# Kernel optimization log

Measured on AMD Instinct MI355X. Metric: run time of the kernel, lower is better.

The kernel has to match this reference:

```python
import jax, jax.numpy as jnp
import numpy as np

HEADS = 8
DIM_HEAD = 64


def setup_inputs() -> dict:
    key = jax.random.key(0)
    ks = jax.random.split(key, 7)
    b, c, h, w = 8, 256, 64, 64
    hidden = HEADS * DIM_HEAD  # 512
    return {
        "x": jax.random.normal(ks[0], (b, c, h, w), dtype=jnp.float32),
        "context": jax.random.normal(ks[1], (b, c, h, w), dtype=jnp.float32),
        "Wq": jax.random.normal(ks[2], (hidden, c), dtype=jnp.float32) * 0.02,
        "Wk": jax.random.normal(ks[3], (hidden, c), dtype=jnp.float32) * 0.02,
        "Wv": jax.random.normal(ks[4], (hidden, c), dtype=jnp.float32) * 0.02,
        "Wo": jax.random.normal(ks[5], (c, hidden), dtype=jnp.float32) * 0.02,
        "bo": jnp.zeros((c,), dtype=jnp.float32),
    }


def reference(x, context, Wq, Wk, Wv, Wo, bo):
    b, c, h, w = x.shape
    n = h * w
    scale = DIM_HEAD ** (-0.5)
    xf = x.reshape(b, c, n)                      # b c n
    cf = context.reshape(b, context.shape[1], -1)  # b c m
    # 1x1 convs == per-pixel linear projections
    q = jnp.einsum('bcn,oc->bon', xf, Wq).reshape(b, HEADS, DIM_HEAD, n) * scale
    k = jnp.einsum('bcm,oc->bom', cf, Wk).reshape(b, HEADS, DIM_HEAD, -1)
    v = jnp.einsum('bcm,oc->bom', cf, Wv).reshape(b, HEADS, DIM_HEAD, -1)
    k = jax.nn.softmax(k, axis=-1)               # softmax over spatial positions
    ctx = jnp.einsum('bhdm,bhem->bhde', k, v)    # small d x e context
    out = jnp.einsum('bhde,bhdn->bhen', ctx, q)  # b h e n
    out = out.reshape(b, HEADS * DIM_HEAD, h, w)
    return jnp.einsum('bchw,oc->bohw', out, Wo) + bo[None, :, None, None]
```

## Files before the change

kernel.cpp:

```cpp
#include <hip/hip_runtime.h>

#define B   8
#define C   256
#define N   4096
#define H   8
#define D   64
#define HID 512
#define SCALE 0.125f

typedef __attribute__((ext_vector_type(8))) __bf16 bf16x8;
typedef __attribute__((ext_vector_type(4))) float f32x4;

__device__ __forceinline__ ushort f2bf(float f) {
  union { float f; unsigned u; } v; v.f = f;
  unsigned r = v.u + 0x7FFFu + ((v.u >> 16) & 1u);
  return (ushort)(r >> 16);
}

__device__ __forceinline__ f32x4 mfma16(bf16x8 a, bf16x8 b, f32x4 c) {
  return __builtin_amdgcn_mfma_f32_16x16x32_bf16(a, b, c, 0, 0, 0);
}

__device__ __forceinline__ void glds16(const ushort* g, ushort* l) {
  __builtin_amdgcn_global_load_lds(
      (const __attribute__((address_space(1))) void*)g,
      (__attribute__((address_space(3))) void*)l, 16, 0, 0);
}

__global__ __launch_bounds__(256) void prep_kernel(
    const float* __restrict__ x, const float* __restrict__ ctxt,
    const float* __restrict__ Wk, const float* __restrict__ Wv,
    ushort* __restrict__ x_bf, ushort* __restrict__ ctxt_bf,
    ushort* __restrict__ wk_bf, ushort* __restrict__ wv_bf) {
  const int z = blockIdx.z;
  const int tid = threadIdx.x;
  if (z == 16) {
    const int id = blockIdx.y * 64 + blockIdx.x;
    if (id >= 128) return;
    const int t = (id * 256 + tid) * 4;
    const float4 a = *(const float4*)(Wk + t);
    const float4 b = *(const float4*)(Wv + t);
    ushort4 ra, rb;
    ra.x = f2bf(a.x); ra.y = f2bf(a.y); ra.z = f2bf(a.z); ra.w = f2bf(a.w);
    rb.x = f2bf(b.x); rb.y = f2bf(b.y); rb.z = f2bf(b.z); rb.w = f2bf(b.w);
    *(ushort4*)(wk_bf + t) = ra;
    *(ushort4*)(wv_bf + t) = rb;
    return;
  }
  __shared__ float tile[64 * 65];
  const int b = z & 7;
  const float* src = (z < 8) ? ctxt : x;
  ushort* dst = (z < 8) ? ctxt_bf : x_bf;
  const int l0 = blockIdx.x * 64, r0 = blockIdx.y * 64;
  const int rr = tid >> 4, c4 = (tid & 15) << 2;
  const float* sp = src + ((size_t)b * C + r0) * N + l0;
#pragma unroll
  for (int p = 0; p < 4; ++p) {
    const float4 v = *(const float4*)(sp + (size_t)(rr + p * 16) * N + c4);
    float* tp = tile + (rr + p * 16) * 65 + c4;
    tp[0] = v.x; tp[1] = v.y; tp[2] = v.z; tp[3] = v.w;
  }
  __syncthreads();
  const int lr = tid >> 2, rb = (tid & 3) << 4;
  uint pk[8];
#pragma unroll
  for (int k = 0; k < 16; k += 2) {
    const uint lo = f2bf(tile[(rb + k) * 65 + lr]);
    const uint hi = f2bf(tile[(rb + k + 1) * 65 + lr]);
    pk[k >> 1] = lo | (hi << 16);
  }
  ushort* dp = dst + ((size_t)b * N + l0 + lr) * C + r0 + rb;
  *(uint4*)dp = *(uint4*)pk;
  *(uint4*)(dp + 8) = *(uint4*)(pk + 4);
}

__global__ __launch_bounds__(256, 4) void kv_mfma_kernel(
    const ushort* __restrict__ ctxt_bf,
    const ushort* __restrict__ wk_bf,
    const ushort* __restrict__ wv_bf,
    float* __restrict__ ctx_part,
    float* __restrict__ z_part)
{
  __shared__ __align__(16) ushort cb_s[2][32 * 256];
  __shared__ __align__(16) ushort p_s[64 * 32];
  __shared__ __align__(16) ushort v_s[64 * 32];
  const int mt = blockIdx.x, h = blockIdx.y, b = blockIdx.z;
  const int tid = threadIdx.x;
  const int w = tid >> 6, lane = tid & 63;
  const int col = lane & 15, quad = lane >> 4;
  const int dw = w * 16;
  const int swc = (col & 3) ^ ((col >> 2) & 3);

  const ushort* wkp = wk_bf + (size_t)(h * 64 + dw + col) * C + quad * 8;
  const ushort* wvp = wv_bf + (size_t)(h * 64 + dw + col) * C + quad * 8;
  const ushort* cbase = ctxt_bf + ((size_t)b * N + (size_t)mt * 256) * C;

  const int grow0 = w * 8 + (lane >> 5);
  const int ggran = lane & 31;

  const f32x4 z4 = {0.f, 0.f, 0.f, 0.f};
  f32x4 cacc[4];
#pragma unroll
  for (int j = 0; j < 4; ++j) cacc[j] = z4;
  float zl = 0.f;

#pragma unroll
  for (int it = 0; it < 4; ++it) {
    const int row = grow0 + it * 2;
    glds16(cbase + (size_t)row * C + ((ggran ^ (row & 7)) << 3),
           &cb_s[0][(w * 8 + it * 2) * 256]);
  }
  __syncthreads();

  for (int t = 0; t < 8; ++t) {
    const int cur = t & 1;
    if (t < 7) {
      const ushort* nb = cbase + (size_t)(t + 1) * 32 * C;
#pragma unroll
      for (int it = 0; it < 4; ++it) {
        const int row = grow0 + it * 2;
        glds16(nb + (size_t)row * C + ((ggran ^ (row & 7)) << 3),
               &cb_s[cur ^ 1][(w * 8 + it * 2) * 256]);
      }
    }

    f32x4 kacc[2], vacc[2];
#pragma unroll
    for (int i = 0; i < 2; ++i) { kacc[i] = z4; vacc[i] = z4; }
#pragma unroll
    for (int kk = 0; kk < 8; ++kk) {
      bf16x8 a[2];
#pragma unroll
      for (int i = 0; i < 2; ++i) {
        const int r = i * 16 + col;
        a[i] = *(const bf16x8*)(&cb_s[cur][r * 256 +
                  ((((kk << 2) + quad) ^ (r & 7)) << 3)]);
      }
      const bf16x8 wkf = *(const bf16x8*)(wkp + (size_t)kk * 32);
      const bf16x8 wvf = *(const bf16x8*)(wvp + (size_t)kk * 32);
#pragma unroll
      for (int i = 0; i < 2; ++i) {
        kacc[i] = mfma16(a[i], wkf, kacc[i]);
        vacc[i] = mfma16(a[i], wvf, vacc[i]);
      }
    }

#pragma unroll
    for (int i = 0; i < 2; ++i) {
      const int off = (dw + col) * 32 +
                      (((i * 2 + (quad >> 1)) ^ swc) << 3) + ((quad & 1) << 2);
      const f32x4 k4 = kacc[i];
      const float e0 = __expf(k4[0]), e1 = __expf(k4[1]);
      const float e2 = __expf(k4[2]), e3 = __expf(k4[3]);
      zl += (e0 + e1) + (e2 + e3);
      ushort4 pk; pk.x = f2bf(e0); pk.y = f2bf(e1);
      pk.z = f2bf(e2); pk.w = f2bf(e3);
      *(ushort4*)(p_s + off) = pk;
      const f32x4 v4 = vacc[i];
      ushort4 vk; vk.x = f2bf(v4[0]); vk.y = f2bf(v4[1]);
      vk.z = f2bf(v4[2]); vk.w = f2bf(v4[3]);
      *(ushort4*)(v_s + off) = vk;
    }
    __syncthreads();

    {
      const int g = (quad ^ swc) << 3;
      const bf16x8 pa = *(const bf16x8*)(p_s + (dw + col) * 32 + g);
      bf16x8 vb[4];
#pragma unroll
      for (int j = 0; j < 4; ++j)
        vb[j] = *(const bf16x8*)(v_s + (j * 16 + col) * 32 + g);
#pragma unroll
      for (int j = 0; j < 4; ++j) cacc[j] = mfma16(pa, vb[j], cacc[j]);
    }
    __syncthreads();
  }

  {
    float s = zl;
    s += __shfl_xor(s, 16); s += __shfl_xor(s, 32);
    if (quad == 0)
      z_part[((size_t)(b * H + h) * 16 + mt) * 64 + dw + col] = s;
  }

  float* outp = ctx_part + ((size_t)(b * H + h) * 16 + mt) * 4096;
#pragma unroll
  for (int j = 0; j < 4; ++j)
#pragma unroll
    for (int r = 0; r < 4; ++r)
      outp[(size_t)(dw + quad * 4 + r) * 64 + j * 16 + col] = cacc[j][r];
}

__global__ __launch_bounds__(256) void a_kernel(
    const float* __restrict__ ctx_part, const float* __restrict__ z_part,
    const float* __restrict__ Wq, float* __restrict__ A)
{
  const int bh = blockIdx.x, cti = blockIdx.y, tid = threadIdx.x;
  const int b = bh >> 3, h = bh & 7;
  const int c0 = cti << 6;
  __shared__ float ct[64 * 65];
  __shared__ float wq[64 * 68];
  __shared__ float zs[64];
  if (tid < 64) {
    float z = 0.f;
#pragma unroll
    for (int p = 0; p < 16; ++p) z += z_part[((size_t)bh * 16 + p) * 64 + tid];
    zs[tid] = SCALE / z;
  }
  __syncthreads();
  const float* cp = ctx_part + (size_t)bh * 16 * 4096;
  for (int r = 0; r < 16; ++r) {
    const int idx = tid + (r << 8);
    float s = 0.f;
#pragma unroll
    for (int p = 0; p < 16; ++p) s += cp[(size_t)p * 4096 + idx];
    ct[(idx & 63) * 65 + (idx >> 6)] = s * zs[idx >> 6];
    wq[(idx >> 6) * 68 + (idx & 63)] =
        Wq[(size_t)(h * 64 + (idx >> 6)) * C + c0 + (idx & 63)];
  }
  __syncthreads();
  const int e = tid & 63, co = tid >> 6;
  float acc[16];
#pragma unroll
  for (int k = 0; k < 16; ++k) acc[k] = 0.f;
  for (int d = 0; d < 64; ++d) {
    const float cv = ct[e * 65 + d];
    const float* wr = wq + d * 68 + co * 16;
#pragma unroll
    for (int k = 0; k < 16; ++k) acc[k] += cv * wr[k];
  }
  float* Ar = A + ((size_t)b * HID + h * 64 + e) * C + c0 + co * 16;
#pragma unroll
  for (int k = 0; k < 16; ++k) Ar[k] = acc[k];
}

__global__ __launch_bounds__(256) void m_kernel(
    const float* __restrict__ A, const float* __restrict__ Wo,
    ushort* __restrict__ M_bf)
{
  const int tile = blockIdx.x, b = blockIdx.y;
  const int o0 = (tile & 7) << 5, c0 = (tile >> 3) << 6;
  const int tid = threadIdx.x, tx = tid & 15, ty = tid >> 4;
  __shared__ float wo_s[64 * 33];
  __shared__ float a_s[64 * 68];
  float acc[2][4] = {{0.f}};
  const int wo_o = tid >> 3, wo_k = (tid & 7) << 3;
  const int a_k = tid >> 2, a_c = (tid & 3) << 4;
  float4 wr0, wr1, ar0, ar1, ar2, ar3;
  {
    const float* wp = Wo + (size_t)(o0 + wo_o) * HID + wo_k;
    wr0 = *(const float4*)wp; wr1 = *(const float4*)(wp + 4);
    const float* ap = A + ((size_t)b * HID + a_k) * C + c0 + a_c;
    ar0 = *(const float4*)ap;       ar1 = *(const float4*)(ap + 4);
    ar2 = *(const float4*)(ap + 8); ar3 = *(const float4*)(ap + 12);
  }
  for (int t = 0; t < 8; ++t) {
    __syncthreads();
    {
      float* wd = wo_s + wo_k * 33 + wo_o;
      wd[0]   = wr0.x; wd[33]  = wr0.y; wd[66]  = wr0.z; wd[99]  = wr0.w;
      wd[132] = wr1.x; wd[165] = wr1.y; wd[198] = wr1.z; wd[231] = wr1.w;
      float* ad = a_s + a_k * 68 + a_c;
      *(float4*)ad = ar0;       *(float4*)(ad + 4) = ar1;
      *(float4*)(ad + 8) = ar2; *(float4*)(ad + 12) = ar3;
    }
    __syncthreads();
    if (t < 7) {
      const int k0 = (t + 1) << 6;
      const float* wp = Wo + (size_t)(o0 + wo_o) * HID + k0 + wo_k;
      wr0 = *(const float4*)wp; wr1 = *(const float4*)(wp + 4);
      const float* ap = A + ((size_t)b * HID + k0 + a_k) * C + c0 + a_c;
      ar0 = *(const float4*)ap;       ar1 = *(const float4*)(ap + 4);
      ar2 = *(const float4*)(ap + 8); ar3 = *(const float4*)(ap + 12);
    }
#pragma unroll
    for (int kc = 0; kc < 64; ++kc) {
      const float2 wv = *(const float2*)(wo_s + kc * 33 + ty * 2);
      const float4 av = *(const float4*)(a_s + kc * 68 + tx * 4);
      acc[0][0] += wv.x * av.x; acc[0][1] += wv.x * av.y;
      acc[0][2] += wv.x * av.z; acc[0][3] += wv.x * av.w;
      acc[1][0] += wv.y * av.x; acc[1][1] += wv.y * av.y;
      acc[1][2] += wv.y * av.z; acc[1][3] += wv.y * av.w;
    }
  }
#pragma unroll
  for (int i = 0; i < 2; ++i) {
    ushort4 r;
    r.x = f2bf(acc[i][0]); r.y = f2bf(acc[i][1]);
    r.z = f2bf(acc[i][2]); r.w = f2bf(acc[i][3]);
    *(ushort4*)(M_bf + ((size_t)b * C + o0 + ty * 2 + i) * C + c0 + tx * 4) = r;
  }
}

__global__ __launch_bounds__(256, 4) void out_mfma_kernel(
    const ushort* __restrict__ M_bf,
    const ushort* __restrict__ x_bf,
    const float* __restrict__ bo, float* __restrict__ out)
{
  const int r = blockIdx.x + 16 * blockIdx.y + 128 * blockIdx.z;
  const int xcd = r & 7, slot = r >> 3;
  const int grp = xcd * 16 + (slot >> 3);
  const int ot = slot & 7;
  const int b = grp >> 4, nt = grp & 15;
  const int tid = threadIdx.x;
  const int w = tid >> 6, lane = tid & 63;
  const int col = lane & 15, quad = lane >> 4;
  const int o0 = ot * 32;
  const size_t n_base = (size_t)nt * 256 + w * 64;
  const ushort* Ab = M_bf + ((size_t)b * C + o0 + col) * C + quad * 8;
  const ushort* Bb = x_bf + ((size_t)b * N + n_base) * C + quad * 8;

  const f32x4 z4 = {0.f, 0.f, 0.f, 0.f};
  f32x4 acc[2][4];
#pragma unroll
  for (int i = 0; i < 2; ++i)
#pragma unroll
    for (int j = 0; j < 4; ++j) acc[i][j] = z4;

#pragma unroll
  for (int kk = 0; kk < 8; ++kk) {
    bf16x8 af[2], bfz[4];
#pragma unroll
    for (int i = 0; i < 2; ++i)
      af[i] = *(const bf16x8*)(Ab + (size_t)(i * 16) * C + kk * 32);
#pragma unroll
    for (int j = 0; j < 4; ++j)
      bfz[j] = *(const bf16x8*)(Bb + (size_t)(j * 16 + col) * C + kk * 32);
#pragma unroll
    for (int i = 0; i < 2; ++i)
#pragma unroll
      for (int j = 0; j < 4; ++j) acc[i][j] = mfma16(af[i], bfz[j], acc[i][j]);
  }

#pragma unroll
  for (int i = 0; i < 2; ++i)
#pragma unroll
    for (int r2 = 0; r2 < 4; ++r2) {
      const int o = o0 + i * 16 + quad * 4 + r2;
      const float bias = bo[o];
      float* op = out + ((size_t)b * C + o) * N + n_base + col;
#pragma unroll
      for (int j = 0; j < 4; ++j) op[j * 16] = acc[i][j][r2] + bias;
    }
}

extern "C" void kernel_launch(void* const* d_in, const int* in_sizes, int n_in,
                              void* d_out, int out_size, void* d_ws, size_t ws_size,
                              hipStream_t stream) {
  const float* x    = (const float*)d_in[0];
  const float* ctxt = (const float*)d_in[1];
  const float* Wq   = (const float*)d_in[2];
  const float* Wk   = (const float*)d_in[3];
  const float* Wv   = (const float*)d_in[4];
  const float* Wo   = (const float*)d_in[5];
  const float* bo   = (const float*)d_in[6];
  float* out = (float*)d_out;

  char* p = (char*)d_ws;
  ushort* ctxt_bf = (ushort*)p;  p += (size_t)B * N * C * 2;
  ushort* x_bf    = (ushort*)p;  p += (size_t)B * N * C * 2;
  ushort* wk_bf   = (ushort*)p;  p += (size_t)HID * C * 2;
  ushort* wv_bf   = (ushort*)p;  p += (size_t)HID * C * 2;
  ushort* M_bf    = (ushort*)p;  p += (size_t)B * C * C * 2;
  float*  z_part  = (float*)p;   p += (size_t)B * H * 16 * 64 * 4;
  float*  A       = (float*)p;   p += (size_t)B * HID * C * 4;
  float*  ctx_part= (float*)p;   p += (size_t)B * H * 16 * 4096 * 4;

  prep_kernel<<<dim3(N / 64, C / 64, 17), 256, 0, stream>>>(
      x, ctxt, Wk, Wv, x_bf, ctxt_bf, wk_bf, wv_bf);
  kv_mfma_kernel<<<dim3(16, H, B), 256, 0, stream>>>(
      ctxt_bf, wk_bf, wv_bf, ctx_part, z_part);
  a_kernel<<<dim3(B * H, 4), 256, 0, stream>>>(ctx_part, z_part, Wq, A);
  m_kernel<<<dim3(32, B), 256, 0, stream>>>(A, Wo, M_bf);
  out_mfma_kernel<<<dim3(N / 256, C / 32, B), 256, 0, stream>>>(M_bf, x_bf, bo, out);
}
```

Baseline: 202.1 us.

## Restructure output GEMM with register-resident M and double-buffered LDS x tiles

The output projection kernel now keeps each wave's 32x256 slice of M in registers and streams x tiles of 32 rows through double-buffered, XOR-swizzled shared memory using global-to-LDS loads. Each block covers 128 output channels and 128 pixels in four steps, so the x loads are shared across the four waves instead of each wave reading x directly from global memory. The XCD-aware block remapping is removed and launch bounds drop to 3 blocks per CU. The cost is higher register pressure and lower occupancy, plus more barriers per block.

```diff
diff --git a/kernel.cpp b/kernel.cpp
--- a/kernel.cpp
+++ b/kernel.cpp
@@ -292,56 +292,94 @@
   }
 }
 
-__global__ __launch_bounds__(256, 4) void out_mfma_kernel(
+__global__ __launch_bounds__(256, 3) void out_mfma_kernel(
     const ushort* __restrict__ M_bf,
     const ushort* __restrict__ x_bf,
     const float* __restrict__ bo, float* __restrict__ out)
 {
-  const int r = blockIdx.x + 16 * blockIdx.y + 128 * blockIdx.z;
-  const int xcd = r & 7, slot = r >> 3;
-  const int grp = xcd * 16 + (slot >> 3);
-  const int ot = slot & 7;
-  const int b = grp >> 4, nt = grp & 15;
+  __shared__ __align__(16) ushort xs[2][32 * 256];
+  const int nt = blockIdx.x;
+  const int ot = blockIdx.y;
+  const int b  = blockIdx.z;
   const int tid = threadIdx.x;
   const int w = tid >> 6, lane = tid & 63;
   const int col = lane & 15, quad = lane >> 4;
-  const int o0 = ot * 32;
-  const size_t n_base = (size_t)nt * 256 + w * 64;
-  const ushort* Ab = M_bf + ((size_t)b * C + o0 + col) * C + quad * 8;
-  const ushort* Bb = x_bf + ((size_t)b * N + n_base) * C + quad * 8;
-
-  const f32x4 z4 = {0.f, 0.f, 0.f, 0.f};
-  f32x4 acc[2][4];
+  const int ow = ot * 128 + w * 32;
+
+  const ushort* xbase = x_bf + ((size_t)b * N + (size_t)nt * 128) * C;
+  const int grow0 = w * 8 + (lane >> 5);
+  const int ggran = lane & 31;
+
+  bf16x8 mf[8][2];
+#pragma unroll
+  for (int kk = 0; kk < 8; ++kk)
+#pragma unroll
+    for (int i = 0; i < 2; ++i)
+      mf[kk][i] = *(const bf16x8*)(M_bf +
+          ((size_t)b * C + ow + i * 16 + col) * C + kk * 32 + quad * 8);
+
+  float bias[2][4];
 #pragma unroll
   for (int i = 0; i < 2; ++i)
 #pragma unroll
-    for (int j = 0; j < 4; ++j) acc[i][j] = z4;
-
-#pragma unroll
-  for (int kk = 0; kk < 8; ++kk) {
-    bf16x8 af[2], bfz[4];
+    for (int r = 0; r < 4; ++r)
+      bias[i][r] = bo[ow + i * 16 + quad * 4 + r];
+
+#pragma unroll
+  for (int it = 0; it < 4; ++it) {
+    const int row = grow0 + it * 2;
+    glds16(xbase + (size_t)row * C + ((ggran ^ (row & 7)) << 3),
+           &xs[0][(w * 8 + it * 2) * 256]);
+  }
+  __syncthreads();
+
+  for (int t = 0; t < 4; ++t) {
+    const int cur = t & 1;
+    if (t < 3) {
+      const ushort* nb = xbase + (size_t)(t + 1) * 32 * C;
+#pragma unroll
+      for (int it = 0; it < 4; ++it) {
+        const int row = grow0 + it * 2;
+        glds16(nb + (size_t)row * C + ((ggran ^ (row & 7)) << 3),
+               &xs[cur ^ 1][(w * 8 + it * 2) * 256]);
+      }
+    }
+
+    const f32x4 z4 = {0.f, 0.f, 0.f, 0.f};
+    f32x4 acc[2][2];
 #pragma unroll
     for (int i = 0; i < 2; ++i)
-      af[i] = *(const bf16x8*)(Ab + (size_t)(i * 16) * C + kk * 32);
-#pragma unroll
-    for (int j = 0; j < 4; ++j)
-      bfz[j] = *(const bf16x8*)(Bb + (size_t)(j * 16 + col) * C + kk * 32);
+#pragma unroll
+      for (int j = 0; j < 2; ++j) acc[i][j] = z4;
+
+#pragma unroll
+    for (int kk = 0; kk < 8; ++kk) {
+      bf16x8 bx[2];
+#pragma unroll
+      for (int j = 0; j < 2; ++j) {
+        const int r = j * 16 + col;
+        bx[j] = *(const bf16x8*)(&xs[cur][r * 256 +
+                  ((((kk << 2) + quad) ^ (r & 7)) << 3)]);
+      }
+#pragma unroll
+      for (int i = 0; i < 2; ++i)
+#pragma unroll
+        for (int j = 0; j < 2; ++j)
+          acc[i][j] = mfma16(mf[kk][i], bx[j], acc[i][j]);
+    }
+
 #pragma unroll
     for (int i = 0; i < 2; ++i)
 #pragma unroll
-      for (int j = 0; j < 4; ++j) acc[i][j] = mfma16(af[i], bfz[j], acc[i][j]);
-  }
-
-#pragma unroll
-  for (int i = 0; i < 2; ++i)
-#pragma unroll
-    for (int r2 = 0; r2 < 4; ++r2) {
-      const int o = o0 + i * 16 + quad * 4 + r2;
-      const float bias = bo[o];
-      float* op = out + ((size_t)b * C + o) * N + n_base + col;
-#pragma unroll
-      for (int j = 0; j < 4; ++j) op[j * 16] = acc[i][j][r2] + bias;
-    }
+      for (int r = 0; r < 4; ++r) {
+        const int o = ow + i * 16 + quad * 4 + r;
+        float* op = out + ((size_t)b * C + o) * N + nt * 128 + t * 32 + col;
+#pragma unroll
+        for (int j = 0; j < 2; ++j)
+          op[j * 16] = acc[i][j][r] + bias[i][r];
+      }
+    __syncthreads();
+  }
 }
 
 extern "C" void kernel_launch(void* const* d_in, const int* in_sizes, int n_in,
@@ -372,5 +410,5 @@
       ctxt_bf, wk_bf, wv_bf, ctx_part, z_part);
   a_kernel<<<dim3(B * H, 4), 256, 0, stream>>>(ctx_part, z_part, Wq, A);
   m_kernel<<<dim3(32, B), 256, 0, stream>>>(A, Wo, M_bf);
-  out_mfma_kernel<<<dim3(N / 256, C / 32, B), 256, 0, stream>>>(M_bf, x_bf, bo, out);
-}
+  out_mfma_kernel<<<dim3(32, 2, B), 256, 0, stream>>>(M_bf, x_bf, bo, out);
+}
```

New measurement: 190.8 us. -5.6%, faster.
